# Optimization experiments

Hardware: AMD Instinct MI355X
Metric: run time of the kernel (lower is better)

The kernel has to match this reference:

```python
import jax, jax.numpy as jnp
import numpy as np

OUTPUT_SIZE = 7
SPATIAL_SCALE = 0.25
SAMPLING_RATIO = 2


def setup_inputs() -> dict:
    key = jax.random.key(0)
    k1, k2, k3, k4, k5 = jax.random.split(key, 5)
    B, C, H, W = 4, 256, 100, 152
    N = 1000
    inp = jax.random.normal(k1, (B, C, H, W), dtype=jnp.float32)
    # image-space canvas is (H/scale, W/scale) = (400, 608); build valid xyxy boxes
    img_h, img_w = H / SPATIAL_SCALE, W / SPATIAL_SCALE
    x1 = jax.random.uniform(k2, (N,), minval=0.0, maxval=img_w - 16.0)
    y1 = jax.random.uniform(k3, (N,), minval=0.0, maxval=img_h - 16.0)
    bw = jax.random.uniform(k4, (N, 2), minval=8.0, maxval=160.0)
    x2 = jnp.minimum(x1 + bw[:, 0], img_w - 1.0)
    y2 = jnp.minimum(y1 + bw[:, 1], img_h - 1.0)
    boxes = jnp.stack([x1, y1, x2, y2], axis=1).astype(jnp.float32)
    box_indices = jax.random.randint(k5, (N,), 0, B, dtype=jnp.int32)
    return {"input": inp, "boxes": boxes, "box_indices": box_indices}


def _roi_align(feat, boxes, box_indices, P, scale, sr):
    # feat: [B,C,H,W], boxes: [N,4] xyxy in image coords, box_indices: [N]
    B, C, H, W = feat.shape
    N = boxes.shape[0]
    S = P * sr  # samples per side

    x1, y1, x2, y2 = [boxes[:, i] * scale for i in range(4)]
    roi_w = jnp.maximum(x2 - x1, 1.0)  # legacy aligned=False: min size 1
    roi_h = jnp.maximum(y2 - y1, 1.0)
    bin_w = roi_w / P
    bin_h = roi_h / P

    # sample s in [0,S): coord = start + bin * (s + 0.5)/sr  (== ph*bin + (iy+0.5)*bin/sr)
    offs = (jnp.arange(S, dtype=feat.dtype) + 0.5) / sr  # [S]
    ys = y1[:, None] + bin_h[:, None] * offs  # [N,S]
    xs = x1[:, None] + bin_w[:, None] * offs  # [N,S]

    valid_y = (ys > -1.0) & (ys < H)  # [N,S]
    valid_x = (xs > -1.0) & (xs < W)
    mask = (valid_y[:, :, None] & valid_x[:, None, :]).astype(feat.dtype)  # [N,S,S]

    yc = jnp.clip(ys, 0.0, H - 1)
    xc = jnp.clip(xs, 0.0, W - 1)
    yl = jnp.floor(yc).astype(jnp.int32)
    xl = jnp.floor(xc).astype(jnp.int32)
    yh = jnp.minimum(yl + 1, H - 1)
    xh = jnp.minimum(xl + 1, W - 1)
    ly = yc - yl  # [N,S]
    lx = xc - xl
    hy = 1.0 - ly
    hx = 1.0 - lx

    b = box_indices[:, None, None]  # [N,1,1]

    def corner(yi, xi):
        # gather [N,S,S,C] from feat[B,C,H,W]
        return feat[b, :, yi[:, :, None], xi[:, None, :]]

    w1 = (hy[:, :, None] * hx[:, None, :] * mask)[..., None]
    w2 = (hy[:, :, None] * lx[:, None, :] * mask)[..., None]
    w3 = (ly[:, :, None] * hx[:, None, :] * mask)[..., None]
    w4 = (ly[:, :, None] * lx[:, None, :] * mask)[..., None]

    vals = (w1 * corner(yl, xl) + w2 * corner(yl, xh)
            + w3 * corner(yh, xl) + w4 * corner(yh, xh))  # [N,S,S,C]

    # average pool sr x sr samples per bin
    pooled = vals.reshape(N, P, sr, P, sr, C).mean(axis=(2, 4))  # [N,P,P,C]
    return jnp.transpose(pooled, (0, 3, 1, 2))  # [N,C,P,P]


def reference(input, boxes, box_indices):
    return _roi_align(input, boxes, box_indices, OUTPUT_SIZE, SPATIAL_SCALE, SAMPLING_RATIO)
```

## Files before the change

kernel.cpp:

```cpp
#include <hip/hip_runtime.h>
#include <hip/hip_bf16.h>

#define BB    4
#define CC    256
#define HH    100
#define WW    152
#define NBOX  1000
#define PB    7
#define SRR   2
#define SCALE 0.25f

__global__ __launch_bounds__(256) void transpose_kernel(
    const float* __restrict__ in, ushort* __restrict__ out)
{
    __shared__ float tile[32][33];
    const int S = HH * WW;
    const int tilesS = S / 32;
    const int tilesC = CC / 32;

    int bid = blockIdx.x;
    int b   = bid / (tilesS * tilesC);
    int r   = bid % (tilesS * tilesC);
    int ts  = r / tilesC;
    int tc  = r % tilesC;
    int s0  = ts * 32, c0 = tc * 32;

    int tx  = threadIdx.x & 31;
    int ty4 = threadIdx.x >> 5;

    #pragma unroll
    for (int i = 0; i < 4; i++) {
        int c = c0 + ty4 * 4 + i;
        int s = s0 + tx;
        tile[ty4 * 4 + i][tx] = in[((size_t)b * CC + c) * S + s];
    }
    __syncthreads();
    #pragma unroll
    for (int i = 0; i < 4; i++) {
        int s = s0 + ty4 * 4 + i;
        int c = c0 + tx;
        __hip_bfloat16 h = __float2bfloat16(tile[tx][ty4 * 4 + i]);
        out[((size_t)b * S + s) * CC + c] = *(ushort*)&h;
    }
}

__global__ __launch_bounds__(512) void roialign_kernel(
    const ushort* __restrict__ feat,
    const float*  __restrict__ boxes,
    const int*    __restrict__ inds,
    float*        __restrict__ out)
{
    __shared__ float lds[128 * PB * PB];

    const int n    = blockIdx.x >> 1;
    const int half = blockIdx.x & 1;
    const int t = threadIdx.x;
    const int w = t >> 6;
    const int l = t & 63;
    const int cl = 2 * l;

    const float x1 = boxes[n * 4 + 0] * SCALE;
    const float y1 = boxes[n * 4 + 1] * SCALE;
    const float x2 = boxes[n * 4 + 2] * SCALE;
    const float y2 = boxes[n * 4 + 3] * SCALE;
    const int   b  = inds[n];

    const float roi_w = fmaxf(x2 - x1, 1.0f);
    const float roi_h = fmaxf(y2 - y1, 1.0f);
    const float bin_w = roi_w * (1.0f / PB);
    const float bin_h = roi_h * (1.0f / PB);

    const ushort* fbase = feat + (size_t)b * (HH * WW * CC) + half * 128 + cl;

    for (int p = w; p < PB * PB; p += 8) {
        const int py = p / PB;
        const int px = p % PB;
        float accx = 0.f, accy = 0.f;
        #pragma unroll
        for (int iy = 0; iy < SRR; iy++) {
            const float yy = y1 + bin_h * (((float)(py * SRR + iy) + 0.5f) * (1.0f / SRR));
            const bool  vy = (yy > -1.0f) && (yy < (float)HH);
            const float ycl = fminf(fmaxf(yy, 0.0f), (float)(HH - 1));
            const int   yl  = (int)ycl;
            const int   yh  = min(yl + 1, HH - 1);
            const float lyf = ycl - (float)yl;
            const float hyf = 1.0f - lyf;
            #pragma unroll
            for (int ix = 0; ix < SRR; ix++) {
                const float xx = x1 + bin_w * (((float)(px * SRR + ix) + 0.5f) * (1.0f / SRR));
                const bool  vx = (xx > -1.0f) && (xx < (float)WW);
                const float m  = (vy && vx) ? 1.0f : 0.0f;
                const float xcl = fminf(fmaxf(xx, 0.0f), (float)(WW - 1));
                const int   xl  = (int)xcl;
                const int   xh  = min(xl + 1, WW - 1);
                const float lxf = xcl - (float)xl;
                const float hxf = 1.0f - lxf;

                const float w11 = m * hyf * hxf;
                const float w12 = m * hyf * lxf;
                const float w21 = m * lyf * hxf;
                const float w22 = m * lyf * lxf;

                const uint v11 = *(const uint*)(fbase + (yl * WW + xl) * CC);
                const uint v12 = *(const uint*)(fbase + (yl * WW + xh) * CC);
                const uint v21 = *(const uint*)(fbase + (yh * WW + xl) * CC);
                const uint v22 = *(const uint*)(fbase + (yh * WW + xh) * CC);

                accx += w11 * __uint_as_float(v11 << 16)
                      + w12 * __uint_as_float(v12 << 16)
                      + w21 * __uint_as_float(v21 << 16)
                      + w22 * __uint_as_float(v22 << 16);
                accy += w11 * __uint_as_float(v11 & 0xFFFF0000u)
                      + w12 * __uint_as_float(v12 & 0xFFFF0000u)
                      + w21 * __uint_as_float(v21 & 0xFFFF0000u)
                      + w22 * __uint_as_float(v22 & 0xFFFF0000u);
            }
        }
        const float inv = 1.0f / (SRR * SRR);
        lds[(cl + 0) * (PB * PB) + p] = accx * inv;
        lds[(cl + 1) * (PB * PB) + p] = accy * inv;
    }

    __syncthreads();
    float4*       out4 = (float4*)(out + ((size_t)n * CC + half * 128) * (PB * PB));
    const float4* lds4 = (const float4*)lds;
    #pragma unroll
    for (int k = t; k < (128 * PB * PB) / 4; k += 512)
        out4[k] = lds4[k];
}

extern "C" void kernel_launch(void* const* d_in, const int* in_sizes, int n_in,
                              void* d_out, int out_size, void* d_ws, size_t ws_size,
                              hipStream_t stream)
{
    const float* feat  = (const float*)d_in[0];
    const float* boxes = (const float*)d_in[1];
    const int*   inds  = (const int*)d_in[2];
    float*       out   = (float*)d_out;

    ushort* ft = (ushort*)d_ws;
    const int tiles = BB * ((HH * WW) / 32) * (CC / 32);
    transpose_kernel<<<tiles, 256, 0, stream>>>(feat, ft);
    roialign_kernel<<<2 * NBOX, 512, 0, stream>>>(ft, boxes, inds, out);
}
```

Before: 51.50 us.

## Sort boxes by batch and Morton spatial key, swizzle blocks across XCDs

Adds a single-block counting-sort kernel that orders boxes by batch index and a 3-bit Morton code of the box centre. The ROI-align grid maps block IDs through this order with an 8-way XCD-style swizzle, so spatially nearby boxes land on the same die and share L2 cache lines of the transposed feature map. The per-position loop is also manually unrolled into a fixed pattern of 6 or 7 positions per wave. This costs an extra kernel launch and an indirection load per block.

```diff
diff --git a/kernel.cpp b/kernel.cpp
--- a/kernel.cpp
+++ b/kernel.cpp
@@ -10,6 +10,49 @@
 #define SRR   2
 #define SCALE 0.25f
 
+__global__ __launch_bounds__(1024) void order_kernel(
+    const float* __restrict__ boxes, const int* __restrict__ inds,
+    int* __restrict__ order)
+{
+    __shared__ unsigned cnt[256];
+    __shared__ unsigned base[256];
+    const int t = threadIdx.x;
+    if (t < 256) cnt[t] = 0;
+    __syncthreads();
+
+    int key = 0;
+    if (t < NBOX) {
+        const float xc = 0.5f * (boxes[t * 4 + 0] + boxes[t * 4 + 2]) * SCALE;
+        const float yc = 0.5f * (boxes[t * 4 + 1] + boxes[t * 4 + 3]) * SCALE;
+        int xq = min((int)(xc * (8.0f / WW)), 7);
+        int yq = min((int)(yc * (8.0f / HH)), 7);
+        xq = max(xq, 0); yq = max(yq, 0);
+        const int m = ((yq >> 2) & 1) << 5 | ((xq >> 2) & 1) << 4 |
+                      ((yq >> 1) & 1) << 3 | ((xq >> 1) & 1) << 2 |
+                      (yq & 1) << 1 | (xq & 1);
+        key = (inds[t] << 6) | m;
+        atomicAdd(&cnt[key], 1u);
+    }
+    __syncthreads();
+    if (t < 256) base[t] = cnt[t];
+    __syncthreads();
+    for (int off = 1; off < 256; off <<= 1) {
+        unsigned v = 0;
+        if (t < 256 && t >= off) v = base[t - off];
+        __syncthreads();
+        if (t < 256) base[t] += v;
+        __syncthreads();
+    }
+    if (t < 256) base[t] -= cnt[t];
+    __syncthreads();
+    if (t < 256) cnt[t] = 0;
+    __syncthreads();
+    if (t < NBOX) {
+        const unsigned p = base[key] + atomicAdd(&cnt[key], 1u);
+        order[p] = t;
+    }
+}
+
 __global__ __launch_bounds__(256) void transpose_kernel(
     const float* __restrict__ in, ushort* __restrict__ out)
 {
@@ -48,16 +91,18 @@
     const ushort* __restrict__ feat,
     const float*  __restrict__ boxes,
     const int*    __restrict__ inds,
+    const int*    __restrict__ order,
     float*        __restrict__ out)
 {
     __shared__ float lds[128 * PB * PB];
 
-    const int n    = blockIdx.x >> 1;
-    const int half = blockIdx.x & 1;
+    const int rank = (blockIdx.x & 7) * (2 * NBOX / 8) + (blockIdx.x >> 3);
+    const int n    = order[rank >> 1];
+    const int half = rank & 1;
+
     const int t = threadIdx.x;
     const int w = t >> 6;
-    const int l = t & 63;
-    const int cl = 2 * l;
+    const int cl = 2 * (t & 63);
 
     const float x1 = boxes[n * 4 + 0] * SCALE;
     const float y1 = boxes[n * 4 + 1] * SCALE;
@@ -71,55 +116,62 @@
     const float bin_h = roi_h * (1.0f / PB);
 
     const ushort* fbase = feat + (size_t)b * (HH * WW * CC) + half * 128 + cl;
-
-    for (int p = w; p < PB * PB; p += 8) {
-        const int py = p / PB;
-        const int px = p % PB;
-        float accx = 0.f, accy = 0.f;
-        #pragma unroll
-        for (int iy = 0; iy < SRR; iy++) {
-            const float yy = y1 + bin_h * (((float)(py * SRR + iy) + 0.5f) * (1.0f / SRR));
-            const bool  vy = (yy > -1.0f) && (yy < (float)HH);
-            const float ycl = fminf(fmaxf(yy, 0.0f), (float)(HH - 1));
-            const int   yl  = (int)ycl;
-            const int   yh  = min(yl + 1, HH - 1);
-            const float lyf = ycl - (float)yl;
-            const float hyf = 1.0f - lyf;
-            #pragma unroll
-            for (int ix = 0; ix < SRR; ix++) {
-                const float xx = x1 + bin_w * (((float)(px * SRR + ix) + 0.5f) * (1.0f / SRR));
-                const bool  vx = (xx > -1.0f) && (xx < (float)WW);
-                const float m  = (vy && vx) ? 1.0f : 0.0f;
-                const float xcl = fminf(fmaxf(xx, 0.0f), (float)(WW - 1));
-                const int   xl  = (int)xcl;
-                const int   xh  = min(xl + 1, WW - 1);
-                const float lxf = xcl - (float)xl;
-                const float hxf = 1.0f - lxf;
-
-                const float w11 = m * hyf * hxf;
-                const float w12 = m * hyf * lxf;
-                const float w21 = m * lyf * hxf;
-                const float w22 = m * lyf * lxf;
-
-                const uint v11 = *(const uint*)(fbase + (yl * WW + xl) * CC);
-                const uint v12 = *(const uint*)(fbase + (yl * WW + xh) * CC);
-                const uint v21 = *(const uint*)(fbase + (yh * WW + xl) * CC);
-                const uint v22 = *(const uint*)(fbase + (yh * WW + xh) * CC);
-
-                accx += w11 * __uint_as_float(v11 << 16)
-                      + w12 * __uint_as_float(v12 << 16)
-                      + w21 * __uint_as_float(v21 << 16)
-                      + w22 * __uint_as_float(v22 << 16);
-                accy += w11 * __uint_as_float(v11 & 0xFFFF0000u)
-                      + w12 * __uint_as_float(v12 & 0xFFFF0000u)
-                      + w21 * __uint_as_float(v21 & 0xFFFF0000u)
-                      + w22 * __uint_as_float(v22 & 0xFFFF0000u);
-            }
-        }
-        const float inv = 1.0f / (SRR * SRR);
-        lds[(cl + 0) * (PB * PB) + p] = accx * inv;
-        lds[(cl + 1) * (PB * PB) + p] = accy * inv;
-    }
+    const float inv = 1.0f / (SRR * SRR);
+
+#define POS_BODY(P)                                                           \
+    {                                                                         \
+        const int py = (P) / PB;                                              \
+        const int px = (P) % PB;                                              \
+        float accx = 0.f, accy = 0.f;                                         \
+        _Pragma("unroll")                                                     \
+        for (int iy = 0; iy < SRR; iy++) {                                    \
+            const float yy = y1 + bin_h * (((float)(py * SRR + iy) + 0.5f) * (1.0f / SRR)); \
+            const bool  vy = (yy > -1.0f) && (yy < (float)HH);                \
+            const float ycl = fminf(fmaxf(yy, 0.0f), (float)(HH - 1));        \
+            const int   yl  = (int)ycl;                                       \
+            const int   yh  = min(yl + 1, HH - 1);                            \
+            const float lyf = ycl - (float)yl;                                \
+            const float hyf = 1.0f - lyf;                                     \
+            _Pragma("unroll")                                                 \
+            for (int ix = 0; ix < SRR; ix++) {                                \
+                const float xx = x1 + bin_w * (((float)(px * SRR + ix) + 0.5f) * (1.0f / SRR)); \
+                const bool  vx = (xx > -1.0f) && (xx < (float)WW);            \
+                const float m  = (vy && vx) ? 1.0f : 0.0f;                    \
+                const float xcl = fminf(fmaxf(xx, 0.0f), (float)(WW - 1));    \
+                const int   xl  = (int)xcl;                                   \
+                const int   xh  = min(xl + 1, WW - 1);                        \
+                const float lxf = xcl - (float)xl;                            \
+                const float hxf = 1.0f - lxf;                                 \
+                const float w11 = m * hyf * hxf;                              \
+                const float w12 = m * hyf * lxf;                              \
+                const float w21 = m * lyf * hxf;                              \
+                const float w22 = m * lyf * lxf;                              \
+                const uint v11 = *(const uint*)(fbase + (yl * WW + xl) * CC); \
+                const uint v12 = *(const uint*)(fbase + (yl * WW + xh) * CC); \
+                const uint v21 = *(const uint*)(fbase + (yh * WW + xl) * CC); \
+                const uint v22 = *(const uint*)(fbase + (yh * WW + xh) * CC); \
+                accx += w11 * __uint_as_float(v11 << 16)                      \
+                      + w12 * __uint_as_float(v12 << 16)                      \
+                      + w21 * __uint_as_float(v21 << 16)                      \
+                      + w22 * __uint_as_float(v22 << 16);                     \
+                accy += w11 * __uint_as_float(v11 & 0xFFFF0000u)              \
+                      + w12 * __uint_as_float(v12 & 0xFFFF0000u)              \
+                      + w21 * __uint_as_float(v21 & 0xFFFF0000u)              \
+                      + w22 * __uint_as_float(v22 & 0xFFFF0000u);             \
+            }                                                                 \
+        }                                                                     \
+        lds[(cl + 0) * (PB * PB) + (P)] = accx * inv;                         \
+        lds[(cl + 1) * (PB * PB) + (P)] = accy * inv;                         \
+    }
+
+    #pragma unroll
+    for (int it = 0; it < 3; it++) {
+        const int p0 = w + 16 * it;
+        POS_BODY(p0);
+        POS_BODY(p0 + 8);
+    }
+    if (w == 0) POS_BODY(48);
+#undef POS_BODY
 
     __syncthreads();
     float4*       out4 = (float4*)(out + ((size_t)n * CC + half * 128) * (PB * PB));
@@ -138,8 +190,11 @@
     const int*   inds  = (const int*)d_in[2];
     float*       out   = (float*)d_out;
 
-    ushort* ft = (ushort*)d_ws;
+    ushort* ft    = (ushort*)d_ws;
+    int*    order = (int*)((char*)d_ws + (size_t)BB * HH * WW * CC * 2);
+
+    order_kernel<<<1, 1024, 0, stream>>>(boxes, inds, order);
     const int tiles = BB * ((HH * WW) / 32) * (CC / 32);
     transpose_kernel<<<tiles, 256, 0, stream>>>(feat, ft);
-    roialign_kernel<<<2 * NBOX, 512, 0, stream>>>(ft, boxes, inds, out);
-}
+    roialign_kernel<<<2 * NBOX, 512, 0, stream>>>(ft, boxes, inds, order, out);
+}
```

Measured after the change: 54.61 us. 1.06x slower.

## Precompute bilinear weights/offsets in LDS, halve block size, swizzle block order

Applied to the files above, without the earlier changes.

Sample weights and corner offsets are now computed once per block by 196 threads and stored in shared memory, instead of being recomputed by every wave. The block shrinks to 256 threads, with each wave handling 12-13 bins in a fully unrolled loop, and the output staging buffer is stored as bf16 to cut LDS use. Block indices are remapped so that consecutive blocks are spread across XCDs. Rounding the pooled output to bf16 before writing it as fp32 adds precision loss.

```diff
diff --git a/kernel.cpp b/kernel.cpp
--- a/kernel.cpp
+++ b/kernel.cpp
@@ -44,89 +44,97 @@
     }
 }
 
-__global__ __launch_bounds__(512) void roialign_kernel(
+__global__ __launch_bounds__(256) void roialign_kernel(
     const ushort* __restrict__ feat,
     const float*  __restrict__ boxes,
     const int*    __restrict__ inds,
     float*        __restrict__ out)
 {
-    __shared__ float lds[128 * PB * PB];
+    __shared__ ushort obuf[128 * PB * PB];
+    __shared__ float4 pw[PB * PB * SRR * SRR];
+    __shared__ int4   po[PB * PB * SRR * SRR];
 
-    const int n    = blockIdx.x >> 1;
-    const int half = blockIdx.x & 1;
-    const int t = threadIdx.x;
-    const int w = t >> 6;
-    const int l = t & 63;
-    const int cl = 2 * l;
+    const int logical = (blockIdx.x & 7) * (2 * NBOX / 8) + (blockIdx.x >> 3);
+    const int n    = logical >> 1;
+    const int half = logical & 1;
 
-    const float x1 = boxes[n * 4 + 0] * SCALE;
-    const float y1 = boxes[n * 4 + 1] * SCALE;
-    const float x2 = boxes[n * 4 + 2] * SCALE;
-    const float y2 = boxes[n * 4 + 3] * SCALE;
-    const int   b  = inds[n];
+    const int t  = threadIdx.x;
+    const int w  = t >> 6;
+    const int cl = 2 * (t & 63);
 
-    const float roi_w = fmaxf(x2 - x1, 1.0f);
-    const float roi_h = fmaxf(y2 - y1, 1.0f);
-    const float bin_w = roi_w * (1.0f / PB);
-    const float bin_h = roi_h * (1.0f / PB);
+    const int b = inds[n];
 
-    const ushort* fbase = feat + (size_t)b * (HH * WW * CC) + half * 128 + cl;
+    if (t < PB * PB * SRR * SRR) {
+        const float x1 = boxes[n * 4 + 0] * SCALE;
+        const float y1 = boxes[n * 4 + 1] * SCALE;
+        const float x2 = boxes[n * 4 + 2] * SCALE;
+        const float y2 = boxes[n * 4 + 3] * SCALE;
+        const float bin_w = fmaxf(x2 - x1, 1.0f) * (1.0f / PB);
+        const float bin_h = fmaxf(y2 - y1, 1.0f) * (1.0f / PB);
+        const int p  = t >> 2;
+        const int s  = t & 3;
+        const int py = p / PB, px = p % PB;
+        const int iy = s >> 1, ix = s & 1;
+        const float yy = y1 + bin_h * (((float)(py * SRR + iy) + 0.5f) * (1.0f / SRR));
+        const float xx = x1 + bin_w * (((float)(px * SRR + ix) + 0.5f) * (1.0f / SRR));
+        const bool  v  = (yy > -1.0f) && (yy < (float)HH) &&
+                         (xx > -1.0f) && (xx < (float)WW);
+        const float m  = v ? (1.0f / (SRR * SRR)) : 0.0f;
+        const float ycl = fminf(fmaxf(yy, 0.0f), (float)(HH - 1));
+        const float xcl = fminf(fmaxf(xx, 0.0f), (float)(WW - 1));
+        const int yl = (int)ycl, xl = (int)xcl;
+        const int yh = min(yl + 1, HH - 1), xh = min(xl + 1, WW - 1);
+        const float ly = ycl - (float)yl, lx = xcl - (float)xl;
+        const float hy = 1.0f - ly,       hx = 1.0f - lx;
+        pw[t] = make_float4(m * hy * hx, m * hy * lx, m * ly * hx, m * ly * lx);
+        po[t] = make_int4((yl * WW + xl) * (CC * 2), (yl * WW + xh) * (CC * 2),
+                          (yh * WW + xl) * (CC * 2), (yh * WW + xh) * (CC * 2));
+    }
+    __syncthreads();
 
-    for (int p = w; p < PB * PB; p += 8) {
-        const int py = p / PB;
-        const int px = p % PB;
-        float accx = 0.f, accy = 0.f;
-        #pragma unroll
-        for (int iy = 0; iy < SRR; iy++) {
-            const float yy = y1 + bin_h * (((float)(py * SRR + iy) + 0.5f) * (1.0f / SRR));
-            const bool  vy = (yy > -1.0f) && (yy < (float)HH);
-            const float ycl = fminf(fmaxf(yy, 0.0f), (float)(HH - 1));
-            const int   yl  = (int)ycl;
-            const int   yh  = min(yl + 1, HH - 1);
-            const float lyf = ycl - (float)yl;
-            const float hyf = 1.0f - lyf;
-            #pragma unroll
-            for (int ix = 0; ix < SRR; ix++) {
-                const float xx = x1 + bin_w * (((float)(px * SRR + ix) + 0.5f) * (1.0f / SRR));
-                const bool  vx = (xx > -1.0f) && (xx < (float)WW);
-                const float m  = (vy && vx) ? 1.0f : 0.0f;
-                const float xcl = fminf(fmaxf(xx, 0.0f), (float)(WW - 1));
-                const int   xl  = (int)xcl;
-                const int   xh  = min(xl + 1, WW - 1);
-                const float lxf = xcl - (float)xl;
-                const float hxf = 1.0f - lxf;
+    const char* fbase = (const char*)feat +
+        ((size_t)b * (HH * WW * CC) + half * 128 + cl) * 2;
 
-                const float w11 = m * hyf * hxf;
-                const float w12 = m * hyf * lxf;
-                const float w21 = m * lyf * hxf;
-                const float w22 = m * lyf * lxf;
+#define LO(u) __uint_as_float((u) << 16)
+#define HI(u) __uint_as_float((u) & 0xFFFF0000u)
 
-                const uint v11 = *(const uint*)(fbase + (yl * WW + xl) * CC);
-                const uint v12 = *(const uint*)(fbase + (yl * WW + xh) * CC);
-                const uint v21 = *(const uint*)(fbase + (yh * WW + xl) * CC);
-                const uint v22 = *(const uint*)(fbase + (yh * WW + xh) * CC);
-
-                accx += w11 * __uint_as_float(v11 << 16)
-                      + w12 * __uint_as_float(v12 << 16)
-                      + w21 * __uint_as_float(v21 << 16)
-                      + w22 * __uint_as_float(v22 << 16);
-                accy += w11 * __uint_as_float(v11 & 0xFFFF0000u)
-                      + w12 * __uint_as_float(v12 & 0xFFFF0000u)
-                      + w21 * __uint_as_float(v21 & 0xFFFF0000u)
-                      + w22 * __uint_as_float(v22 & 0xFFFF0000u);
-            }
-        }
-        const float inv = 1.0f / (SRR * SRR);
-        lds[(cl + 0) * (PB * PB) + p] = accx * inv;
-        lds[(cl + 1) * (PB * PB) + p] = accy * inv;
+#define POS_BODY(P)                                                           \
+    {                                                                         \
+        float a0 = 0.f, a1 = 0.f;                                             \
+        _Pragma("unroll")                                                     \
+        for (int s = 0; s < 4; s++) {                                         \
+            const float4 wv = pw[(P) * 4 + s];            \
+            const int4   ov = po[(P) * 4 + s];            \
+            const uint u0 = *(const uint*)(fbase + ov.x);                     \
+            const uint u1 = *(const uint*)(fbase + ov.y);                     \
+            const uint u2 = *(const uint*)(fbase + ov.z);                     \
+            const uint u3 = *(const uint*)(fbase + ov.w);                     \
+            a0 += wv.x * LO(u0) + wv.y * LO(u1) + wv.z * LO(u2) + wv.w * LO(u3); \
+            a1 += wv.x * HI(u0) + wv.y * HI(u1) + wv.z * HI(u2) + wv.w * HI(u3); \
+        }                                                                     \
+        __hip_bfloat16 h0 = __float2bfloat16(a0);                             \
+        __hip_bfloat16 h1 = __float2bfloat16(a1);                             \
+        obuf[(cl + 0) * (PB * PB) + (P)] = *(ushort*)&h0;                     \
+        obuf[(cl + 1) * (PB * PB) + (P)] = *(ushort*)&h1;                     \
     }
 
+    #pragma unroll
+    for (int i = 0; i < 6; i++) {
+        POS_BODY(w + 8 * i);
+        POS_BODY(w + 8 * i + 4);
+    }
+    if (w == 0) POS_BODY(48);
+#undef POS_BODY
+
     __syncthreads();
-    float4*       out4 = (float4*)(out + ((size_t)n * CC + half * 128) * (PB * PB));
-    const float4* lds4 = (const float4*)lds;
-    #pragma unroll
-    for (int k = t; k < (128 * PB * PB) / 4; k += 512)
-        out4[k] = lds4[k];
+    const uint2* l2   = (const uint2*)obuf;
+    float4*      out4 = (float4*)(out + ((size_t)n * CC + half * 128) * (PB * PB));
+    for (int k = t; k < 128 * PB * PB / 4; k += 256) {
+        const uint2 v = l2[k];
+        out4[k] = make_float4(LO(v.x), HI(v.x), LO(v.y), HI(v.y));
+    }
+#undef LO
+#undef HI
 }
 
 extern "C" void kernel_launch(void* const* d_in, const int* in_sizes, int n_in,
@@ -141,5 +149,5 @@
     ushort* ft = (ushort*)d_ws;
     const int tiles = BB * ((HH * WW) / 32) * (CC / 32);
     transpose_kernel<<<tiles, 256, 0, stream>>>(feat, ft);
-    roialign_kernel<<<2 * NBOX, 512, 0, stream>>>(ft, boxes, inds, out);
+    roialign_kernel<<<2 * NBOX, 256, 0, stream>>>(ft, boxes, inds, out);
 }
```

After: 51.79 us. About the same (+0.6%).
